# Kernel optimization log

Measured on AMD Instinct MI355X. Metric: run time of the kernel, lower is better.

## Reference

```python
import jax, jax.numpy as jnp
import numpy as np

PC_RANGE = np.array([-40.0, -40.0, -1.0, 40.0, 40.0, 5.4], np.float32)
RADIUS = 39.0
STEP_SIZE = 0.5
WORLD_LEN = 200
NUM_CLASSES = 17
FAST_THRES = 1e-7
W_ENT = 0.01
W_DIST = 0.01
W_SEM = 1.0
ALPHA_INIT = 1e-6

_xyz_min_w = PC_RANGE[:3]
_xyz_max_w = PC_RANGE[3:]
_rng = _xyz_max_w - _xyz_min_w
BG_LEN = float((np.floor_divide(_rng[0], 2.0) - RADIUS) / RADIUS)
SCENE_CENTER = ((_xyz_min_w + _xyz_max_w) * 0.5).astype(np.float32)
_Z = float(_rng[2] / _rng[0])
XYZ_MIN = np.array([-1.0 - BG_LEN, -1.0 - BG_LEN, -_Z], np.float32)
XYZ_MAX = np.array([1.0 + BG_LEN, 1.0 + BG_LEN, _Z], np.float32)
ACT_SHIFT = float(np.log(1.0 / (1.0 - ALPHA_INIT) - 1.0))
DIST_THRES = (2.0 + 2.0 * BG_LEN) / WORLD_LEN * STEP_SIZE * 0.95

N_INNER = int(2.0 / (2.0 + 2.0 * BG_LEN) * WORLD_LEN / STEP_SIZE) + 1
N_OUTER = N_INNER // 15
_b_in = np.linspace(0.0, 2.0, N_INNER + 1)
_b_out = 2.0 / np.linspace(1.0, 1.0 / 64.0, N_OUTER + 1)
T_VALS = np.concatenate([(_b_in[1:] + _b_in[:-1]) * 0.5, (_b_out[1:] + _b_out[:-1]) * 0.5]).astype(np.float32)

_freq = np.array([1163161, 2309034, 188743, 2997643, 20317180, 852476, 243808, 2457947, 497017, 2731022, 7224789, 214411435, 5565043, 63191967, 76098082, 128860031, 141625221], np.float64)
CLASS_W = (1.0 / np.log(_freq + 0.001)).astype(np.float32)


def trilinear(vol, g):
    # vol: [X,Y,Z,C]; g: [P,3] fractional voxel indices (align_corners=True, zeros padding)
    sizes = jnp.array(vol.shape[:3])
    g0f = jnp.floor(g)
    frac = g - g0f
    g0 = g0f.astype(jnp.int32)
    out = jnp.zeros((g.shape[0], vol.shape[3]), vol.dtype)
    for dx in (0, 1):
        for dy in (0, 1):
            for dz in (0, 1):
                off = jnp.array([dx, dy, dz])
                idx = g0 + off
                w = jnp.prod(jnp.where(off == 1, frac, 1.0 - frac), axis=-1)
                valid = jnp.all((idx >= 0) & (idx < sizes), axis=-1)
                ic = jnp.clip(idx, 0, sizes - 1)
                v = vol[ic[:, 0], ic[:, 1], ic[:, 2]]
                out = out + (w * valid)[:, None] * v
    return out


def _render_losses(density_b, semantic_b, rays_b, bda_b):
    t = jnp.asarray(T_VALS)  # [S]
    gt_depth = rays_b[:, 2]
    gt_depth = jnp.where(gt_depth > 52.0, 0.0, gt_depth)
    ray_valid = gt_depth > 0.0  # [N]
    gt_sem = rays_b[:, 3].astype(jnp.int32)
    ro = rays_b[:, 4:7]
    rd = rays_b[:, 7:10]
    rays_o = (ro - SCENE_CENTER) / RADIUS
    rays_d = rd / jnp.linalg.norm(rd, axis=-1, keepdims=True)
    pts = rays_o[:, None, :] + rays_d[:, None, :] * t[None, :, None]  # [N,S,3]
    nrm = jnp.linalg.norm(pts, axis=-1, keepdims=True)
    inner = (nrm <= 1.0)[..., 0]
    pts = jnp.where(nrm <= 1.0, pts, pts / nrm * (1.0 + BG_LEN - BG_LEN / nrm))
    pts = jnp.einsum('ij,nsj->nsi', bda_b, pts)
    # cumdist_thres: sequential cumulative-distance scan per ray (keep outer points spaced > thres)
    dist = jnp.linalg.norm(pts[:, 1:] - pts[:, :-1], axis=-1)  # [N,S-1]
    def step(cum, d):
        cum = cum + d
        over = cum > DIST_THRES
        return jnp.where(over, 0.0, cum), over
    _, over = jax.lax.scan(step, jnp.zeros(pts.shape[0], pts.dtype), dist.T)
    keep = jnp.concatenate([inner[:, :1], inner[:, 1:] | over.T], axis=1)
    # trilinear grid sample (align_corners=True)
    g = (pts - XYZ_MIN) / (XYZ_MAX - XYZ_MIN)
    gi = (g * (jnp.array([200.0, 200.0, 16.0]) - 1.0)).reshape(-1, 3)
    dens = trilinear(density_b[..., None], gi)[:, 0].reshape(pts.shape[:2])  # [N,S]
    sem = trilinear(semantic_b, gi).reshape(pts.shape[0], pts.shape[1], NUM_CLASSES)  # [N,S,C]
    # Raw2Alpha with interval=0.5: alpha = 1 - (1+exp(d+shift))^(-interval)
    alpha = 1.0 - jnp.power(1.0 + jnp.exp(dens + ACT_SHIFT), -0.5)
    alpha = jnp.where(keep & ray_valid[:, None], alpha, 0.0)
    alpha = jnp.where(alpha > FAST_THRES, alpha, 0.0)  # fast_color_thres cull
    # Alphas2Weights: per-ray exclusive transmittance cumprod
    om = 1.0 - alpha
    Tinc = jnp.cumprod(om, axis=1)
    Texcl = jnp.concatenate([jnp.ones_like(Tinc[:, :1]), Tinc[:, :-1]], axis=1)
    weights = alpha * Texcl
    alphainv_last = Tinc[:, -1]
    pk = weights > FAST_THRES
    w = jnp.where(pk, weights, 0.0)
    # segment_coo semantic render (segment-sum over step dim)
    sem_r = jnp.einsum('ns,nsc->nc', w, sem)
    logp = jax.nn.log_softmax(sem_r, axis=-1)
    nll = -jnp.take_along_axis(logp, gt_sem[:, None], axis=1)[:, 0]
    cw = jnp.asarray(CLASS_W)
    wy = cw[gt_sem] * ray_valid.astype(cw.dtype)
    loss_sem = jnp.sum(wy * nll) / jnp.maximum(jnp.sum(wy), 1e-12)
    # entropy of last transmittance over valid rays
    p = jnp.clip(alphainv_last, 1e-6, 1.0 - 1e-6)
    ent = -(p * jnp.log(p) + (1.0 - p) * jnp.log(1.0 - p))
    nv = jnp.maximum(jnp.sum(ray_valid), 1)
    loss_ent = jnp.sum(jnp.where(ray_valid, ent, 0.0)) / nv
    # flatten_eff_distloss with interval = 1/n_max
    s = 1.0 - 1.0 / (1.0 + t)
    m = jnp.broadcast_to(s[None, :], w.shape)
    n_max = jnp.maximum(jnp.sum(pk), 1)
    interval = 1.0 / n_max
    wm = w * m
    wp = jnp.cumsum(w, axis=1) - w
    wmp = jnp.cumsum(wm, axis=1) - wm
    loss_bi = 2.0 * w * (m * wp - wmp)
    loss_uni = (1.0 / 3.0) * interval * w * w
    loss_dist = (jnp.sum(loss_bi) + jnp.sum(loss_uni)) / nv
    return W_SEM * loss_sem, W_ENT * loss_ent, W_DIST * loss_dist


def setup_inputs():
    key = jax.random.key(0)
    ks = jax.random.split(key, 6)
    B, N = 1, 8192
    density = jax.random.normal(ks[0], (B, 200, 200, 16), jnp.float32)
    semantic = jax.random.normal(ks[1], (B, 200, 200, 16, 17), jnp.float32)
    depth = jax.random.uniform(ks[2], (B, N), jnp.float32, 0.1, 60.0)
    sem_lbl = jax.random.randint(ks[3], (B, N), 0, 17).astype(jnp.float32)
    ro = jax.random.normal(ks[4], (B, N, 3), jnp.float32) + jnp.array([0.0, 0.0, 1.5])
    rd = jax.random.normal(ks[5], (B, N, 3), jnp.float32)
    rd = rd / jnp.linalg.norm(rd, axis=-1, keepdims=True)
    rays = jnp.concatenate([jnp.zeros((B, N, 2)), depth[..., None], sem_lbl[..., None], ro, rd], axis=-1)
    bda = jnp.broadcast_to(jnp.eye(3, dtype=jnp.float32), (B, 3, 3))
    return {"density": density, "semantic": semantic, "rays": rays, "bda": bda}


def reference(density, semantic, rays, bda):
    B = density.shape[0]
    ls, le, ld = 0.0, 0.0, 0.0
    for b in range(B):
        a, c, d = _render_losses(density[b], semantic[b], rays[b], bda[b])
        ls, le, ld = ls + a, le + c, ld + d
    return (ls / B, le / B, ld / B)
```

## Files before the change

kernel.cpp:

```cpp
#include <hip/hip_runtime.h>
#include <math.h>


#define DXX 200
#define DYY 200
#define DZZ 16
#define NC 17
#define S_TOT 416
#define N_IN 390
#define CHUNKS 7
#define NBINS 8
#define BINSTRIDE 16

typedef float v4u __attribute__((ext_vector_type(4), aligned(4), may_alias));
typedef float v2u __attribute__((ext_vector_type(2), aligned(4), may_alias));

__constant__ double c_freq[NC] = {1163161.0, 2309034.0, 188743.0, 2997643.0,
  20317180.0, 852476.0, 243808.0, 2457947.0, 497017.0, 2731022.0, 7224789.0,
  214411435.0, 5565043.0, 63191967.0, 76098082.0, 128860031.0, 141625221.0};

__device__ __forceinline__ float iscan_add(float x, int lane) {
#pragma unroll
  for (int off = 1; off < 64; off <<= 1) {
    float y = __shfl_up(x, off);
    if (lane >= off) x += y;
  }
  return x;
}
__device__ __forceinline__ float iscan_mul(float x, int lane) {
#pragma unroll
  for (int off = 1; off < 64; off <<= 1) {
    float y = __shfl_up(x, off);
    if (lane >= off) x *= y;
  }
  return x;
}

__global__ __launch_bounds__(256) void nerf_zero(float* acc) {
  if (threadIdx.x < NBINS * BINSTRIDE) acc[threadIdx.x] = 0.f;
}

__global__ __launch_bounds__(64) void nerf_main(
    const float* __restrict__ density,
    const float* __restrict__ semantic,
    const float* __restrict__ rays,
    const float* __restrict__ bda,
    float* __restrict__ acc_g,
    int nrays) {
  __shared__ float s_t[CHUNKS * 64];
  __shared__ float s_dist[S_TOT];
  __shared__ unsigned long long s_keep[CHUNKS];
  __shared__ unsigned long long s_big[CHUNKS];

  const int lane = threadIdx.x;
  const int ray = blockIdx.x;
  if (ray >= nrays) return;

  const double BG = (double)(1.0f / 39.0f);
  const float BGf = (float)BG;
  const float DTH = (float)((2.0 + 2.0 * BG) / 200.0 * 0.5 * 0.95);
  const float xminf = (float)(-1.0 - BG);
  const float zf = 6.4f / 80.0f;
  const float sxy = 199.0f / ((float)(1.0 + BG) - xminf);
  const float szc = 15.0f / (zf + zf);
  const float ACTS = -13.815509557964274f;

  const float* rp = rays + (size_t)ray * 10;
  float dep = rp[2];
  if (!((dep > 0.f) && (dep <= 52.f))) return;
  int ysem = (int)rp[3];
  ysem = ysem < 0 ? 0 : (ysem > NC - 1 ? NC - 1 : ysem);
  const float czc = (-1.0f + 5.4f) * 0.5f;
  float rox = rp[4] / 39.0f;
  float roy = rp[5] / 39.0f;
  float roz = (rp[6] - czc) / 39.0f;
  float d0 = rp[7], d1 = rp[8], d2 = rp[9];
  float rn = sqrtf(d0 * d0 + d1 * d1 + d2 * d2);
  float rdx = d0 / rn, rdy = d1 / rn, rdz = d2 / rn;

  for (int i = lane; i < CHUNKS * 64; i += 64) {
    double td;
    if (i < N_IN) {
      td = (2.0 * i + 1.0) / 390.0;
    } else {
      int j = i - N_IN;
      const double stp = (1.0 / 64.0 - 1.0) / 26.0;
      double l0 = 1.0 + j * stp;
      double l1 = (j + 1 >= 26) ? (1.0 / 64.0) : (1.0 + (j + 1) * stp);
      td = 1.0 / l0 + 1.0 / l1;
    }
    s_t[i] = (float)td;
  }
  asm volatile("s_waitcnt lgkmcnt(0)" ::: "memory");

  const float b00 = bda[0], b01 = bda[1], b02 = bda[2];
  const float b10 = bda[3], b11 = bda[4], b12 = bda[5];
  const float b20 = bda[6], b21 = bda[7], b22 = bda[8];

  auto compute_pt = [&](int s, float& tx, float& ty, float& tz, float& tt,
                        bool& inner) {
    tt = s_t[s];
    float qx = rox + rdx * tt;
    float qy = roy + rdy * tt;
    float qz = roz + rdz * tt;
    float nr = sqrtf(qx * qx + qy * qy + qz * qz);
    inner = (nr <= 1.0f) && (s < S_TOT);
    if (nr > 1.0f) {
      float sc = (1.0f + BGf - BGf / nr) / nr;
      qx *= sc; qy *= sc; qz *= sc;
    }
    tx = b00 * qx + b01 * qy + b02 * qz;
    ty = b10 * qx + b11 * qy + b12 * qz;
    tz = b20 * qx + b21 * qy + b22 * qz;
  };

  for (int c = 0; c < CHUNKS; c++) {
    int s = c * 64 + lane;
    float tx, ty, tz, tt; bool inner;
    compute_pt(s, tx, ty, tz, tt, inner);
    unsigned long long bal = __ballot(inner);
    float nx = __shfl(tx, lane + 1);
    float ny = __shfl(ty, lane + 1);
    float nz = __shfl(tz, lane + 1);
    if (c < CHUNKS - 1) {
      float hx, hy, hz, ht; bool hi;
      compute_pt((c + 1) * 64, hx, hy, hz, ht, hi);
      if (lane == 63) { nx = hx; ny = hy; nz = hz; }
    }
    float ex = nx - tx, ey = ny - ty, ez = nz - tz;
    float dd = sqrtf(ex * ex + ey * ey + ez * ez);
    bool dlive = (s < S_TOT - 1);
    if (dlive) s_dist[s] = dd;
    unsigned long long db = __ballot(dlive && (dd > DTH));
    if (lane == 0) { s_keep[c] = bal; s_big[c] = db; }
  }

  asm volatile("s_waitcnt lgkmcnt(0)" ::: "memory");
  if (lane == 0) {
    float cum = 0.f;
    int prev = 0;
    unsigned long long carrybit = 0;
#pragma unroll
    for (int c = 0; c < CHUNKS; c++) {
      unsigned long long inner = s_keep[c];
      unsigned long long db = s_big[c];
      unsigned long long big = (db << 1) | carrybit;
      carrybit = db >> 63;
      unsigned long long valid = ~0ull;
      if (c == 0) valid &= ~1ull;
      if (c == CHUNKS - 1) valid &= 0x00000000FFFFFFFFull;
      big &= valid;
      unsigned long long k = inner | big;
      unsigned long long nb = valid & ~big;
      while (nb) {
        int b = __ffsll((unsigned long long)nb) - 1;
        nb &= nb - 1;
        int s = c * 64 + b;
        if (s - 1 != prev) cum = 0.f;
        cum += s_dist[s - 1];
        if (cum > DTH) { cum = 0.f; k |= 1ull << b; }
        prev = s;
      }
      s_keep[c] = k;
    }
  }
  asm volatile("s_waitcnt lgkmcnt(0)" ::: "memory");

  float out_sem[NC];
#pragma unroll
  for (int j = 0; j < NC; j++) out_sem[j] = 0.f;
  float carry = 1.f, carryW = 0.f, carryWM = 0.f;
  float sum_bi = 0.f, sum_w2 = 0.f, pkcf = 0.f;

  for (int c = 0; c < CHUNKS; c++) {
    unsigned long long km = s_keep[c];
    if (km == 0ull) continue;
    int s = c * 64 + lane;
    float tx, ty, tz, tt; bool inner;
    compute_pt(s, tx, ty, tz, tt, inner);
    float m_ = 1.0f - 1.0f / (1.0f + tt);
    bool keep = (km >> lane) & 1ull;

    float gx = (tx - xminf) * sxy;
    float gy = (ty - xminf) * sxy;
    float gz = (tz + zf) * szc;
    float hxf = floorf(gx), hyf = floorf(gy), hzf = floorf(gz);
    int ix = (int)hxf, iy = (int)hyf, iz = (int)hzf;
    float fx = gx - hxf, fy = gy - hyf, fz = gz - hzf;
    float wx0 = 1.f - fx, wy0 = 1.f - fy, wz0 = 1.f - fz;
    bool vx0 = (unsigned)ix < (unsigned)DXX, vx1 = (unsigned)(ix + 1) < (unsigned)DXX;
    bool vy0 = (unsigned)iy < (unsigned)DYY, vy1 = (unsigned)(iy + 1) < (unsigned)DYY;
    bool vz0 = (unsigned)iz < (unsigned)DZZ, vz1 = (unsigned)(iz + 1) < (unsigned)DZZ;

    float a = 0.f;
    if (keep) {
      float dens = 0.f;
      const float* p0 = density + (ix * DYY + iy) * DZZ + iz;
      if (vx0 && vx1 && vy0 && vy1 && vz0 && vz1) {
        v2u d00 = *(const v2u*)(p0);
        v2u d01 = *(const v2u*)(p0 + DZZ);
        v2u d10 = *(const v2u*)(p0 + DYY * DZZ);
        v2u d11 = *(const v2u*)(p0 + DYY * DZZ + DZZ);
        dens += wx0 * wy0 * wz0 * d00[0];
        dens += wx0 * wy0 * fz  * d00[1];
        dens += wx0 * fy  * wz0 * d01[0];
        dens += wx0 * fy  * fz  * d01[1];
        dens += fx  * wy0 * wz0 * d10[0];
        dens += fx  * wy0 * fz  * d10[1];
        dens += fx  * fy  * wz0 * d11[0];
        dens += fx  * fy  * fz  * d11[1];
      } else {
        if (vx0 && vy0 && vz0) dens += wx0 * wy0 * wz0 * p0[0];
        if (vx0 && vy0 && vz1) dens += wx0 * wy0 * fz  * p0[1];
        if (vx0 && vy1 && vz0) dens += wx0 * fy  * wz0 * p0[DZZ];
        if (vx0 && vy1 && vz1) dens += wx0 * fy  * fz  * p0[DZZ + 1];
        if (vx1 && vy0 && vz0) dens += fx  * wy0 * wz0 * p0[DYY * DZZ];
        if (vx1 && vy0 && vz1) dens += fx  * wy0 * fz  * p0[DYY * DZZ + 1];
        if (vx1 && vy1 && vz0) dens += fx  * fy  * wz0 * p0[DYY * DZZ + DZZ];
        if (vx1 && vy1 && vz1) dens += fx  * fy  * fz  * p0[DYY * DZZ + DZZ + 1];
      }
      float u = expf(dens + ACTS);
      a = -expm1f(-0.5f * log1pf(u));
      if (!(a > 1e-7f)) a = 0.f;
    }

    float om = 1.f - a;
    float ip = iscan_mul(om, lane);
    float ex = __shfl_up(ip, 1); if (lane == 0) ex = 1.f;
    float wgt = a * carry * ex;
    carry *= __shfl(ip, 63);
    float w = (wgt > 1e-7f) ? wgt : 0.f;
    if (w > 0.f) pkcf += 1.f;

    float wm = w * m_;
    float isw = iscan_add(w, lane);
    float iswm = iscan_add(wm, lane);
    float exw = __shfl_up(isw, 1);  if (lane == 0) exw = 0.f;
    float exwm = __shfl_up(iswm, 1); if (lane == 0) exwm = 0.f;
    sum_bi += 2.f * w * (m_ * (carryW + exw) - (carryWM + exwm));
    sum_w2 += w * w;
    carryW += __shfl(isw, 63);
    carryWM += __shfl(iswm, 63);

    if (w > 0.f) {
      const float* sp0 = semantic + (size_t)((ix * DYY + iy) * DZZ + iz) * NC;
      const float* sp1 = sp0 + DYY * DZZ * NC;
#define SEM_ACC(PTR, WC)                                                        \
      { float wc = (WC);                                                        \
        const v4u* q = (const v4u*)(PTR);                                       \
        v4u q0 = q[0], q1 = q[1], q2 = q[2], q3 = q[3];                         \
        float qs = (PTR)[16];                                                   \
        out_sem[0]  += wc * q0[0];  out_sem[1]  += wc * q0[1];                  \
        out_sem[2]  += wc * q0[2];  out_sem[3]  += wc * q0[3];                  \
        out_sem[4]  += wc * q1[0];  out_sem[5]  += wc * q1[1];                  \
        out_sem[6]  += wc * q1[2];  out_sem[7]  += wc * q1[3];                  \
        out_sem[8]  += wc * q2[0];  out_sem[9]  += wc * q2[1];                  \
        out_sem[10] += wc * q2[2];  out_sem[11] += wc * q2[3];                  \
        out_sem[12] += wc * q3[0];  out_sem[13] += wc * q3[1];                  \
        out_sem[14] += wc * q3[2];  out_sem[15] += wc * q3[3];                  \
        out_sem[16] += wc * qs; }
      if (vx0 && vx1 && vy0 && vy1 && vz0 && vz1) {
        SEM_ACC(sp0,                 w * wx0 * wy0 * wz0)
        SEM_ACC(sp0 + NC,            w * wx0 * wy0 * fz)
        SEM_ACC(sp0 + DZZ * NC,      w * wx0 * fy  * wz0)
        SEM_ACC(sp0 + DZZ * NC + NC, w * wx0 * fy  * fz)
        SEM_ACC(sp1,                 w * fx  * wy0 * wz0)
        SEM_ACC(sp1 + NC,            w * fx  * wy0 * fz)
        SEM_ACC(sp1 + DZZ * NC,      w * fx  * fy  * wz0)
        SEM_ACC(sp1 + DZZ * NC + NC, w * fx  * fy  * fz)
      } else {
        if (vx0 && vy0 && vz0) SEM_ACC(sp0,                 w * wx0 * wy0 * wz0)
        if (vx0 && vy0 && vz1) SEM_ACC(sp0 + NC,            w * wx0 * wy0 * fz)
        if (vx0 && vy1 && vz0) SEM_ACC(sp0 + DZZ * NC,      w * wx0 * fy  * wz0)
        if (vx0 && vy1 && vz1) SEM_ACC(sp0 + DZZ * NC + NC, w * wx0 * fy  * fz)
        if (vx1 && vy0 && vz0) SEM_ACC(sp1,                 w * fx  * wy0 * wz0)
        if (vx1 && vy0 && vz1) SEM_ACC(sp1 + NC,            w * fx  * wy0 * fz)
        if (vx1 && vy1 && vz0) SEM_ACC(sp1 + DZZ * NC,      w * fx  * fy  * wz0)
        if (vx1 && vy1 && vz1) SEM_ACC(sp1 + DZZ * NC + NC, w * fx  * fy  * fz)
      }
#undef SEM_ACC
    }
  }

  float r0 = sum_bi, r1 = sum_w2, r2 = pkcf;
#pragma unroll
  for (int off = 32; off >= 1; off >>= 1) {
    r0 += __shfl_xor(r0, off);
    r1 += __shfl_xor(r1, off);
    r2 += __shfl_xor(r2, off);
#pragma unroll
    for (int j = 0; j < NC; j++) out_sem[j] += __shfl_xor(out_sem[j], off);
  }
  if (lane == 0) {
    float M = out_sem[0];
#pragma unroll
    for (int j = 1; j < NC; j++) M = fmaxf(M, out_sem[j]);
    float se = 0.f;
#pragma unroll
    for (int j = 0; j < NC; j++) se += expf(out_sem[j] - M);
    float lse = M + logf(se);
    float sy = 0.f;
#pragma unroll
    for (int j = 0; j < NC; j++) if (j == ysem) sy = out_sem[j];
    float nll = lse - sy;
    float cw = (float)(1.0 / log(c_freq[ysem] + 0.001));
    float p = fminf(fmaxf(carry, 1e-6f), 1.0f - 1e-6f);
    float ent = -(p * logf(p) + (1.f - p) * logf(1.f - p));
    float* bin = acc_g + (ray & (NBINS - 1)) * BINSTRIDE;
    atomicAdd(&bin[0], cw * nll);
    atomicAdd(&bin[1], cw);
    atomicAdd(&bin[2], ent);
    atomicAdd(&bin[3], 1.f);
    atomicAdd(&bin[4], r0);
    atomicAdd(&bin[5], r1);
    atomicAdd(&bin[6], r2);
  }
}

__global__ __launch_bounds__(64) void nerf_fin(const float* __restrict__ acc,
                                               float* __restrict__ out) {
  if (threadIdx.x == 0) {
    float t0 = 0.f, t1 = 0.f, t2 = 0.f, t3 = 0.f, t4 = 0.f, t5 = 0.f, t6 = 0.f;
#pragma unroll
    for (int b = 0; b < NBINS; b++) {
      const float* p = acc + b * BINSTRIDE;
      t0 += p[0]; t1 += p[1]; t2 += p[2]; t3 += p[3];
      t4 += p[4]; t5 += p[5]; t6 += p[6];
    }
    float ls = t0 / fmaxf(t1, 1e-12f);
    float nv = fmaxf(t3, 1.f);
    float le = t2 / nv;
    float nmax = fmaxf(t6, 1.f);
    float ld = (t4 + (1.f / 3.f) * (1.f / nmax) * t5) / nv;
    out[0] = 1.0f * ls;
    out[1] = 0.01f * le;
    out[2] = 0.01f * ld;
  }
}

extern "C" void kernel_launch(void* const* d_in, const int* in_sizes, int n_in,
                              void* d_out, int out_size, void* d_ws, size_t ws_size,
                              hipStream_t stream) {
  const float* density = (const float*)d_in[0];
  const float* semantic = (const float*)d_in[1];
  const float* rays = (const float*)d_in[2];
  const float* bda = (const float*)d_in[3];
  float* out = (float*)d_out;
  float* acc = (float*)d_ws;
  int nrays = in_sizes[2] / 10;
  nerf_zero<<<1, 256, 0, stream>>>(acc);
  nerf_main<<<nrays, 64, 0, stream>>>(density, semantic, rays, bda, acc, nrays);
  nerf_fin<<<1, 64, 0, stream>>>(acc, out);
}
```

Baseline: 321.0 us.

## Reorder rays so long horizontal rays launch first and precompute sample table

Adds a pre-pass kernel that builds a ray permutation, placing valid near-horizontal rays (likely to have many inner samples) at the front and invalid and other rays at the back, so the main kernel schedules its heaviest blocks first and the tail is less imbalanced. The t-value table is now computed once in the zero kernel in double precision and copied into shared memory by each block, instead of every block recomputing it. It adds an extra launch, atomics, and an indirection read per block, and relies on the workspace being large enough to hold the permutation.

```diff
diff --git a/kernel.cpp b/kernel.cpp
--- a/kernel.cpp
+++ b/kernel.cpp
@@ -11,6 +11,9 @@
 #define CHUNKS 7
 #define NBINS 8
 #define BINSTRIDE 16
+#define T_OFF 128
+#define CNT_OFF 1024
+#define PERM_OFF 1088
 
 typedef float v4u __attribute__((ext_vector_type(4), aligned(4), may_alias));
 typedef float v2u __attribute__((ext_vector_type(2), aligned(4), may_alias));
@@ -36,8 +39,43 @@
   return x;
 }
 
-__global__ __launch_bounds__(256) void nerf_zero(float* acc) {
-  if (threadIdx.x < NBINS * BINSTRIDE) acc[threadIdx.x] = 0.f;
+__global__ __launch_bounds__(512) void nerf_zero(float* acc, int nrays) {
+  int i = threadIdx.x;
+  if (i < NBINS * BINSTRIDE) acc[i] = 0.f;
+  if (i < CHUNKS * 64) {
+    double td;
+    if (i < N_IN) {
+      td = (2.0 * i + 1.0) / 390.0;
+    } else {
+      int j = i - N_IN;
+      const double stp = (1.0 / 64.0 - 1.0) / 26.0;
+      double l0 = 1.0 + j * stp;
+      double l1 = (j + 1 >= 26) ? (1.0 / 64.0) : (1.0 + (j + 1) * stp);
+      td = 1.0 / l0 + 1.0 / l1;
+    }
+    acc[T_OFF + i] = (float)td;
+  }
+  if (i == 0) {
+    ((int*)acc)[CNT_OFF] = 0;
+    ((int*)acc)[CNT_OFF + 1] = nrays - 1;
+  }
+}
+
+__global__ __launch_bounds__(256) void nerf_order(
+    const float* __restrict__ rays, int* __restrict__ permbase, int nrays) {
+  int r = blockIdx.x * blockDim.x + threadIdx.x;
+  if (r >= nrays) return;
+  const float* rp = rays + (size_t)r * 10;
+  float dep = rp[2];
+  bool valid = (dep > 0.f) && (dep <= 52.f);
+  float d0 = rp[7], d1 = rp[8], d2 = rp[9];
+  float rn = sqrtf(d0 * d0 + d1 * d1 + d2 * d2);
+  float az = (rn > 0.f) ? fabsf(d2) / rn : 1.f;
+  int* cnts = permbase + CNT_OFF;
+  int* perm = permbase + PERM_OFF;
+  bool lng = valid && (az < 0.10f);
+  int slot = lng ? atomicAdd(&cnts[0], 1) : atomicAdd(&cnts[1], -1);
+  perm[slot] = r;
 }
 
 __global__ __launch_bounds__(64) void nerf_main(
@@ -46,6 +84,7 @@
     const float* __restrict__ rays,
     const float* __restrict__ bda,
     float* __restrict__ acc_g,
+    const int* __restrict__ perm,
     int nrays) {
   __shared__ float s_t[CHUNKS * 64];
   __shared__ float s_dist[S_TOT];
@@ -53,8 +92,9 @@
   __shared__ unsigned long long s_big[CHUNKS];
 
   const int lane = threadIdx.x;
-  const int ray = blockIdx.x;
+  int ray = blockIdx.x;
   if (ray >= nrays) return;
+  if (perm) ray = perm[ray];
 
   const double BG = (double)(1.0f / 39.0f);
   const float BGf = (float)BG;
@@ -78,19 +118,9 @@
   float rn = sqrtf(d0 * d0 + d1 * d1 + d2 * d2);
   float rdx = d0 / rn, rdy = d1 / rn, rdz = d2 / rn;
 
-  for (int i = lane; i < CHUNKS * 64; i += 64) {
-    double td;
-    if (i < N_IN) {
-      td = (2.0 * i + 1.0) / 390.0;
-    } else {
-      int j = i - N_IN;
-      const double stp = (1.0 / 64.0 - 1.0) / 26.0;
-      double l0 = 1.0 + j * stp;
-      double l1 = (j + 1 >= 26) ? (1.0 / 64.0) : (1.0 + (j + 1) * stp);
-      td = 1.0 / l0 + 1.0 / l1;
-    }
-    s_t[i] = (float)td;
-  }
+  const float* g_t = acc_g + T_OFF;
+#pragma unroll
+  for (int i = 0; i < CHUNKS; i++) s_t[i * 64 + lane] = g_t[i * 64 + lane];
   asm volatile("s_waitcnt lgkmcnt(0)" ::: "memory");
 
   const float b00 = bda[0], b01 = bda[1], b02 = bda[2];
@@ -348,7 +378,15 @@
   float* out = (float*)d_out;
   float* acc = (float*)d_ws;
   int nrays = in_sizes[2] / 10;
-  nerf_zero<<<1, 256, 0, stream>>>(acc);
-  nerf_main<<<nrays, 64, 0, stream>>>(density, semantic, rays, bda, acc, nrays);
+  size_t need = (size_t)(PERM_OFF + nrays) * sizeof(int);
+  bool use_perm = ws_size >= need;
+  nerf_zero<<<1, 512, 0, stream>>>(acc, nrays);
+  const int* perm = nullptr;
+  if (use_perm) {
+    nerf_order<<<(nrays + 255) / 256, 256, 0, stream>>>(rays, (int*)acc, nrays);
+    perm = (const int*)acc + PERM_OFF;
+  }
+  nerf_main<<<nrays, 64, 0, stream>>>(density, semantic, rays, bda, acc, perm,
+                                      nrays);
   nerf_fin<<<1, 64, 0, stream>>>(acc, out);
 }
```

Measured after the change: 392.7 us. 1.22x slower.
